# Optimization experiments

Measured on AMD Instinct MI355X. Metric: run time of the kernel, lower is better.

Reference implementation:

```python
import jax, jax.numpy as jnp
import numpy as np

HEADS = 8
DIM_HEAD = 64
SCALE = DIM_HEAD ** (-0.5)


def setup_inputs() -> dict:
    key = jax.random.key(0)
    k1, k2, k3, k4 = jax.random.split(key, 4)
    B, H, W, n, dim = 2, 64, 64, 8, 512
    inner = HEADS * DIM_HEAD  # 512
    x = jax.random.normal(k1, (B, H, W, n, dim), dtype=jnp.float32)
    mask = jax.random.uniform(k2, (B, H, W, 1, n, n), dtype=jnp.float32)
    w_qkv = jax.random.normal(k3, (dim, 3 * inner), dtype=jnp.float32) * 0.02
    w_out = jax.random.normal(k4, (inner, dim), dtype=jnp.float32) * 0.02
    b_out = jnp.zeros((dim,), dtype=jnp.float32)
    return {"x": x, "mask": mask, "w_qkv": w_qkv, "w_out": w_out, "b_out": b_out}


def reference(x, mask, w_qkv, w_out, b_out):
    B, H, W, n, dim = x.shape
    inner = HEADS * DIM_HEAD
    qkv = x @ w_qkv  # [B,H,W,n,3*inner]
    q, k, v = jnp.split(qkv, 3, axis=-1)

    def to_heads(t):
        # 'B H W n (h d) -> B H W h n d'
        t = t.reshape(B, H, W, n, HEADS, DIM_HEAD)
        return jnp.swapaxes(t, 3, 4)

    q, k, v = to_heads(q), to_heads(k), to_heads(v)
    dots = jnp.einsum('bxyhnd,bxyhmd->bxyhnm', q, k) * SCALE
    dots = dots * mask  # multiplicative mask pre-softmax
    attn = jax.nn.softmax(dots, axis=-1)
    out = jnp.einsum('bxyhnm,bxyhmd->bxyhnd', attn, v)
    # 'B H W h n d -> B H W n (h d)'
    out = jnp.swapaxes(out, 3, 4).reshape(B, H, W, n, inner)
    return out @ w_out + b_out
```

## Files before the change

### kernel.cpp

```cpp
#include <hip/hip_runtime.h>
#include <hip/hip_bf16.h>

#define NROWS 65536
#define DIM   512
#define SCALE_ 0.125f

typedef short bf16x8 __attribute__((ext_vector_type(8)));
typedef unsigned short u16x8 __attribute__((ext_vector_type(8)));
typedef float f32x4 __attribute__((ext_vector_type(4)));

__device__ __forceinline__ unsigned short f2bf(float f) {
  union { float f; unsigned u; } v; v.f = f;
  unsigned r = v.u + 0x7FFFu + ((v.u >> 16) & 1u);
  return (unsigned short)(r >> 16);
}

#define GLL16(gptr, lptr) \
  __builtin_amdgcn_global_load_lds((const __attribute__((address_space(1))) void*)(gptr), \
                                   (__attribute__((address_space(3))) void*)(lptr), 16, 0, 0)
#define VMCNT(n) asm volatile("s_waitcnt vmcnt(" #n ")" ::: "memory")
#define LGKM0    asm volatile("s_waitcnt lgkmcnt(0)" ::: "memory")

__global__ void prep_kernel(const float* __restrict__ x,
                            const float* __restrict__ wqkv,
                            const float* __restrict__ wout,
                            unsigned short* __restrict__ xb,
                            unsigned short* __restrict__ wqkvT,
                            unsigned short* __restrict__ woutT) {
  if (blockIdx.x < 16384) {
    size_t i = ((size_t)blockIdx.x * 256 + threadIdx.x) * 8;
    float4 a = *(const float4*)(x + i);
    float4 b = *(const float4*)(x + i + 4);
    u16x8 p;
    p[0] = f2bf(a.x); p[1] = f2bf(a.y); p[2] = f2bf(a.z); p[3] = f2bf(a.w);
    p[4] = f2bf(b.x); p[5] = f2bf(b.y); p[6] = f2bf(b.z); p[7] = f2bf(b.w);
    *(u16x8*)(xb + i) = p;
  } else {
    int idx = (blockIdx.x - 16384) * 256 + threadIdx.x;
    if (idx < 1536 * 512) {
      int j = idx >> 9, c = idx & 511;
      wqkvT[idx] = f2bf(wqkv[(size_t)c * 1536 + j]);
    } else {
      int k2 = idx - 1536 * 512;
      int n = k2 >> 9, c = k2 & 511;
      woutT[k2] = f2bf(wout[(size_t)c * 512 + n]);
    }
  }
}

__global__ __launch_bounds__(256, 2)
void qkv_attn_kernel(const unsigned short* __restrict__ xb,
                     const float* __restrict__ mask,
                     const unsigned short* __restrict__ wqkvT,
                     unsigned short* __restrict__ attn_out) {
  __shared__ __align__(16) unsigned char smem[62464];

  const int t = threadIdx.x;
  const int lane = t & 63, wave = t >> 6;
  const int wm = wave >> 1, wn = wave & 1;
  const int fr = lane & 15, fq = lane >> 4;
  const int l8 = lane >> 3;
  const int cswz = ((lane & 7) ^ l8) * 8;

  const int per = gridDim.x >> 3;
  const int lin = (blockIdx.x & 7) * per + (blockIdx.x >> 3);
  const int mtile = lin >> 3, head = lin & 7;
  const int r0 = mtile * 128;

  f32x4 acc[4][6];
  const f32x4 z4 = {0.f, 0.f, 0.f, 0.f};
  #pragma unroll
  for (int m = 0; m < 4; ++m)
    #pragma unroll
    for (int n = 0; n < 6; ++n) acc[m][n] = z4;

  auto LOAD_A = [&](bf16x8 (&a)[8], int kt2) {
    const unsigned short* g = xb + (size_t)(r0 + wm * 64 + fr) * 512 + kt2 * 64 + fq * 8;
    #pragma unroll
    for (int m = 0; m < 4; ++m)
      #pragma unroll
      for (int kk = 0; kk < 2; ++kk)
        a[m * 2 + kk] = *(const bf16x8*)(g + (size_t)m * 16 * 512 + kk * 32);
  };
  auto STAGE_B = [&](int buf, int kt2) {
    unsigned char* base = smem + buf * 24576;
    const unsigned short* gB = wqkvT + kt2 * 64 + cswz;
    #pragma unroll
    for (int i = 0; i < 6; ++i) {
      int c = wave * 6 + i;
      int n = c * 8 + l8;
      int jg = ((n >> 6) << 9) + head * 64 + (n & 63);
      GLL16(gB + (size_t)jg * 512, base + c * 1024);
    }
  };
  auto COMPUTE = [&](int buf, bf16x8 (&a)[8]) {
    unsigned char* Bb = smem + buf * 24576;
    #pragma unroll
    for (int kk = 0; kk < 2; ++kk) {
      const unsigned ko = ((unsigned)(kk * 64 + fq * 16)) ^ (((unsigned)(fr & 7)) << 4);
      bf16x8 b[6];
      #pragma unroll
      for (int n = 0; n < 6; ++n)
        b[n] = *(const bf16x8*)(Bb + (unsigned)(wn * 96 + n * 16 + fr) * 128 + ko);
      #pragma unroll
      for (int m = 0; m < 4; ++m)
        #pragma unroll
        for (int n = 0; n < 6; ++n)
          acc[m][n] = __builtin_amdgcn_mfma_f32_16x16x32_bf16(a[m * 2 + kk], b[n], acc[m][n], 0, 0, 0);
    }
  };

  bf16x8 aA[8], aB[8];
  LOAD_A(aA, 0);
  STAGE_B(0, 0);
  #pragma unroll
  for (int kt = 0; kt < 8; ++kt) {
    bf16x8 (&aCur)[8] = (kt & 1) ? aB : aA;
    bf16x8 (&aNxt)[8] = (kt & 1) ? aA : aB;
    if (kt < 7) {
      LOAD_A(aNxt, kt + 1);
      STAGE_B((kt + 1) & 1, kt + 1);
      VMCNT(11);
    } else {
      VMCNT(0);
    }
    __builtin_amdgcn_s_barrier();
    COMPUTE(kt & 1, aCur);
    __builtin_amdgcn_s_barrier();
  }

  unsigned short* Qs = (unsigned short*)smem;
  unsigned short* Ks = (unsigned short*)(smem + 16384);
  unsigned short* VT = (unsigned short*)(smem + 32768);
  unsigned short* Pl = (unsigned short*)(smem + 52224);

  float mreg[2][4];
  #pragma unroll
  for (int pp = 0; pp < 2; ++pp) {
    int pair = wave * 2 + pp;
    #pragma unroll
    for (int r = 0; r < 4; ++r) {
      int row = fq * 4 + r;
      int Pg = mtile * 16 + pair * 2 + (row >> 3);
      mreg[pp][r] = mask[(size_t)Pg * 64 + (row & 7) * 8 + (fr & 7)];
    }
  }

  {
    int d = t >> 2, q = t & 3;
    ushort4 z; z.x = 0; z.y = 0; z.z = 0; z.w = 0;
    *(ushort4*)(VT + d * 152 + 128 + q * 4) = z;
  }
  #pragma unroll
  for (int n = 0; n < 6; ++n) {
    int col = wn * 96 + n * 16 + fr;
    #pragma unroll
    for (int m = 0; m < 4; ++m) {
      if (col < 128) {
        unsigned short* T = (col < 64) ? Qs : Ks;
        unsigned cc = (unsigned)(col & 63);
        #pragma unroll
        for (int r = 0; r < 4; ++r) {
          int row = wm * 64 + m * 16 + fq * 4 + r;
          unsigned byte = (unsigned)row * 128 + ((cc * 2) ^ (((unsigned)(row & 7)) << 4));
          *(unsigned short*)((unsigned char*)T + byte) = f2bf(acc[m][n][r]);
        }
      } else {
        int d = col - 128;
        ushort4 p;
        p.x = f2bf(acc[m][n][0]); p.y = f2bf(acc[m][n][1]);
        p.z = f2bf(acc[m][n][2]); p.w = f2bf(acc[m][n][3]);
        *(ushort4*)(VT + d * 152 + (wm * 64 + m * 16 + fq * 4)) = p;
      }
    }
  }
  __syncthreads();

  #pragma unroll
  for (int pp = 0; pp < 2; ++pp) {
    const int pair = wave * 2 + pp;
    const unsigned rbyte = (unsigned)(pair * 16 + fr) * 128;
    const unsigned xrp = ((unsigned)(fr & 7)) << 4;
    f32x4 s = {0.f, 0.f, 0.f, 0.f};
    #pragma unroll
    for (int kk = 0; kk < 2; ++kk) {
      const unsigned ko = ((unsigned)(kk * 64 + fq * 16)) ^ xrp;
      bf16x8 qf = *(const bf16x8*)((unsigned char*)Qs + rbyte + ko);
      bf16x8 kf = *(const bf16x8*)((unsigned char*)Ks + rbyte + ko);
      s = __builtin_amdgcn_mfma_f32_16x16x32_bf16(qf, kf, s, 0, 0, 0);
    }
    float p4[4];
    #pragma unroll
    for (int r = 0; r < 4; ++r) {
      int row = fq * 4 + r;
      bool valid = (row >> 3) == (fr >> 3);
      p4[r] = valid ? s[r] * SCALE_ * mreg[pp][r] : -3.0e38f;
    }
    #pragma unroll
    for (int r = 0; r < 4; ++r) {
      float v = p4[r];
      float mx = v;
      mx = fmaxf(mx, __shfl_xor(mx, 1));
      mx = fmaxf(mx, __shfl_xor(mx, 2));
      mx = fmaxf(mx, __shfl_xor(mx, 4));
      float e = __expf(v - mx);
      float sm = e;
      sm += __shfl_xor(sm, 1);
      sm += __shfl_xor(sm, 2);
      sm += __shfl_xor(sm, 4);
      p4[r] = e / sm;
    }
    #pragma unroll
    for (int r = 0; r < 4; ++r) {
      int row = fq * 4 + r;
      bool valid = (row >> 3) == (fr >> 3);
      Pl[pair * 640 + row * 40 + fr] = valid ? f2bf(p4[r]) : (unsigned short)0;
      Pl[pair * 640 + row * 40 + 16 + fr] = 0;
    }
    #pragma unroll
    for (int dblk = 0; dblk < 4; ++dblk) {
      bf16x8 af = *(const bf16x8*)((unsigned char*)VT +
                    (unsigned)(dblk * 16 + fr) * 304 + (unsigned)(pair * 32 + fq * 16));
      bf16x8 bf = *(const bf16x8*)((unsigned char*)Pl +
                    (unsigned)pair * 1280 + (unsigned)fr * 80 + (unsigned)fq * 16);
      f32x4 o = {0.f, 0.f, 0.f, 0.f};
      o = __builtin_amdgcn_mfma_f32_16x16x32_bf16(af, bf, o, 0, 0, 0);
      ushort4 pk;
      pk.x = f2bf(o[0]); pk.y = f2bf(o[1]); pk.z = f2bf(o[2]); pk.w = f2bf(o[3]);
      *(ushort4*)(attn_out + (size_t)(r0 + pair * 16 + fr) * 512 +
                  head * 64 + dblk * 16 + fq * 4) = pk;
    }
  }
}

__global__ __launch_bounds__(256, 2)
void outproj_kernel(const unsigned short* __restrict__ attn,
                    const unsigned short* __restrict__ woutT,
                    const float* __restrict__ bias,
                    float* __restrict__ out) {
  __shared__ __align__(16) unsigned char smem[65536];
  const int t = threadIdx.x;
  const int lane = t & 63, wave = t >> 6;
  const int wm = wave >> 1, wn = wave & 1;
  const int fr = lane & 15, fq = lane >> 4;
  const int l8 = lane >> 3;
  const int cswz = ((lane & 7) ^ l8) * 8;

  const int per = gridDim.x >> 3;
  const int lin = (blockIdx.x & 7) * per + (blockIdx.x >> 3);
  const int mtile = lin >> 2, nt = lin & 3;
  const int r0 = mtile * 128, n0 = nt * 128;

  f32x4 acc[4][4];
  const f32x4 z4 = {0.f, 0.f, 0.f, 0.f};
  #pragma unroll
  for (int m = 0; m < 4; ++m)
    #pragma unroll
    for (int n = 0; n < 4; ++n) acc[m][n] = z4;

  auto STAGE = [&](int buf, int kt2) {
    unsigned char* base = smem + buf * 32768;
    const int k0 = kt2 * 64;
    const unsigned short* gA = attn  + (size_t)(r0 + l8) * 512 + k0 + cswz;
    const unsigned short* gB = woutT + (size_t)(n0 + l8) * 512 + k0 + cswz;
    #pragma unroll
    for (int i = 0; i < 4; ++i) {
      int c = wave * 4 + i;
      GLL16(gA + (size_t)c * 8 * 512, base + c * 1024);
      GLL16(gB + (size_t)c * 8 * 512, base + 16384 + c * 1024);
    }
  };

  STAGE(0, 0);
  VMCNT(0);
  __syncthreads();
  int cur = 0;

  for (int kt = 0; kt < 8; ++kt) {
    if (kt < 7) STAGE(cur ^ 1, kt + 1);
    unsigned char* Ab = smem + cur * 32768;
    unsigned char* Bb = Ab + 16384;
    const unsigned xr = ((unsigned)(fr & 7)) << 4;
    #pragma unroll
    for (int kk = 0; kk < 2; ++kk) {
      const unsigned ko = ((unsigned)(kk * 64 + fq * 16)) ^ xr;
      bf16x8 a[4], b[4];
      #pragma unroll
      for (int m = 0; m < 4; ++m)
        a[m] = *(const bf16x8*)(Ab + (unsigned)(wm * 64 + m * 16 + fr) * 128 + ko);
      #pragma unroll
      for (int n = 0; n < 4; ++n)
        b[n] = *(const bf16x8*)(Bb + (unsigned)(wn * 64 + n * 16 + fr) * 128 + ko);
      #pragma unroll
      for (int m = 0; m < 4; ++m)
        #pragma unroll
        for (int n = 0; n < 4; ++n)
          acc[m][n] = __builtin_amdgcn_mfma_f32_16x16x32_bf16(a[m], b[n], acc[m][n], 0, 0, 0);
    }
    VMCNT(0);
    __syncthreads();
    cur ^= 1;
  }
  #pragma unroll
  for (int n = 0; n < 4; ++n) {
    int col = n0 + wn * 64 + n * 16 + fr;
    float bv = bias[col];
    #pragma unroll
    for (int m = 0; m < 4; ++m) {
      #pragma unroll
      for (int j = 0; j < 4; ++j) {
        int row = r0 + wm * 64 + m * 16 + fq * 4 + j;
        out[(size_t)row * 512 + col] = acc[m][n][j] + bv;
      }
    }
  }
}

extern "C" void kernel_launch(void* const* d_in, const int* in_sizes, int n_in,
                              void* d_out, int out_size, void* d_ws, size_t ws_size,
                              hipStream_t stream) {
  const float* x    = (const float*)d_in[0];
  const float* mask = (const float*)d_in[1];
  const float* wqkv = (const float*)d_in[2];
  const float* wout = (const float*)d_in[3];
  const float* bias = (const float*)d_in[4];
  float* out = (float*)d_out;

  unsigned char* ws = (unsigned char*)d_ws;
  unsigned short* attn  = (unsigned short*)ws;
  unsigned short* wqkvT = (unsigned short*)(ws + 67108864);
  unsigned short* woutT = (unsigned short*)(ws + 67108864 + 1572864);
  unsigned short* xb    = (unsigned short*)(ws + 67108864 + 1572864 + 524288);

  prep_kernel<<<20480, 256, 0, stream>>>(x, wqkv, wout, xb, wqkvT, woutT);
  qkv_attn_kernel<<<4096, 256, 0, stream>>>(xb, mask, wqkvT, attn);
  outproj_kernel<<<2048, 256, 0, stream>>>(attn, woutT, bias, out);
}
```

Measured before the change: 279.8 us.

## Stage QKV A tiles through LDS and coalesce output GEMM epilogue via shared memory

In the fused QKV+attention kernel, the A operand (x in bf16) now goes to LDS through global_load_lds alongside B, replacing direct per-lane register loads with register double-buffering. Shared memory grows to 80 KB, which may limit occupancy to one or two blocks per CU. The mask loads move earlier so their latency overlaps the GEMM. The output-projection epilogue now goes through a swizzled LDS tile, so each row is written with coalesced float4 stores plus vectorized bias, in place of scattered scalar stores.

```diff
diff --git a/kernel.cpp b/kernel.cpp
--- a/kernel.cpp
+++ b/kernel.cpp
@@ -18,8 +18,7 @@
 #define GLL16(gptr, lptr) \
   __builtin_amdgcn_global_load_lds((const __attribute__((address_space(1))) void*)(gptr), \
                                    (__attribute__((address_space(3))) void*)(lptr), 16, 0, 0)
-#define VMCNT(n) asm volatile("s_waitcnt vmcnt(" #n ")" ::: "memory")
-#define LGKM0    asm volatile("s_waitcnt lgkmcnt(0)" ::: "memory")
+#define VMCNT0 asm volatile("s_waitcnt vmcnt(0)" ::: "memory")
 
 __global__ void prep_kernel(const float* __restrict__ x,
                             const float* __restrict__ wqkv,
@@ -53,7 +52,7 @@
                      const float* __restrict__ mask,
                      const unsigned short* __restrict__ wqkvT,
                      unsigned short* __restrict__ attn_out) {
-  __shared__ __align__(16) unsigned char smem[62464];
+  __shared__ __align__(16) unsigned char smem[81920];
 
   const int t = threadIdx.x;
   const int lane = t & 63, wave = t >> 6;
@@ -67,6 +66,18 @@
   const int mtile = lin >> 3, head = lin & 7;
   const int r0 = mtile * 128;
 
+  float mreg[2][4];
+  #pragma unroll
+  for (int pp = 0; pp < 2; ++pp) {
+    int pair = wave * 2 + pp;
+    #pragma unroll
+    for (int r = 0; r < 4; ++r) {
+      int row = fq * 4 + r;
+      int Pg = mtile * 16 + pair * 2 + (row >> 3);
+      mreg[pp][r] = mask[(size_t)Pg * 64 + (row & 7) * 8 + (fr & 7)];
+    }
+  }
+
   f32x4 acc[4][6];
   const f32x4 z4 = {0.f, 0.f, 0.f, 0.f};
   #pragma unroll
@@ -74,31 +85,42 @@
     #pragma unroll
     for (int n = 0; n < 6; ++n) acc[m][n] = z4;
 
-  auto LOAD_A = [&](bf16x8 (&a)[8], int kt2) {
-    const unsigned short* g = xb + (size_t)(r0 + wm * 64 + fr) * 512 + kt2 * 64 + fq * 8;
-    #pragma unroll
-    for (int m = 0; m < 4; ++m)
-      #pragma unroll
-      for (int kk = 0; kk < 2; ++kk)
-        a[m * 2 + kk] = *(const bf16x8*)(g + (size_t)m * 16 * 512 + kk * 32);
-  };
-  auto STAGE_B = [&](int buf, int kt2) {
-    unsigned char* base = smem + buf * 24576;
-    const unsigned short* gB = wqkvT + kt2 * 64 + cswz;
+  auto STAGE = [&](int buf, int kt2) {
+    unsigned char* base = smem + buf * 40960;
+    const int k0 = kt2 * 64;
+    const unsigned short* gA = xb + (size_t)(r0 + l8) * 512 + k0 + cswz;
+    #pragma unroll
+    for (int i = 0; i < 4; ++i) {
+      int c = wave * 4 + i;
+      GLL16(gA + (size_t)c * 8 * 512, base + c * 1024);
+    }
+    const unsigned short* gB = wqkvT + k0 + cswz;
     #pragma unroll
     for (int i = 0; i < 6; ++i) {
       int c = wave * 6 + i;
       int n = c * 8 + l8;
       int jg = ((n >> 6) << 9) + head * 64 + (n & 63);
-      GLL16(gB + (size_t)jg * 512, base + c * 1024);
+      GLL16(gB + (size_t)jg * 512, base + 16384 + c * 1024);
     }
   };
-  auto COMPUTE = [&](int buf, bf16x8 (&a)[8]) {
-    unsigned char* Bb = smem + buf * 24576;
+
+  STAGE(0, 0);
+  VMCNT0;
+  __syncthreads();
+  int cur = 0;
+
+  for (int kt = 0; kt < 8; ++kt) {
+    if (kt < 7) STAGE(cur ^ 1, kt + 1);
+    unsigned char* Ab = smem + cur * 40960;
+    unsigned char* Bb = Ab + 16384;
+    const unsigned xr = ((unsigned)(fr & 7)) << 4;
     #pragma unroll
     for (int kk = 0; kk < 2; ++kk) {
-      const unsigned ko = ((unsigned)(kk * 64 + fq * 16)) ^ (((unsigned)(fr & 7)) << 4);
-      bf16x8 b[6];
+      const unsigned ko = ((unsigned)(kk * 64 + fq * 16)) ^ xr;
+      bf16x8 a[4], b[6];
+      #pragma unroll
+      for (int m = 0; m < 4; ++m)
+        a[m] = *(const bf16x8*)(Ab + (unsigned)(wm * 64 + m * 16 + fr) * 128 + ko);
       #pragma unroll
       for (int n = 0; n < 6; ++n)
         b[n] = *(const bf16x8*)(Bb + (unsigned)(wn * 96 + n * 16 + fr) * 128 + ko);
@@ -106,45 +128,17 @@
       for (int m = 0; m < 4; ++m)
         #pragma unroll
         for (int n = 0; n < 6; ++n)
-          acc[m][n] = __builtin_amdgcn_mfma_f32_16x16x32_bf16(a[m * 2 + kk], b[n], acc[m][n], 0, 0, 0);
-    }
-  };
-
-  bf16x8 aA[8], aB[8];
-  LOAD_A(aA, 0);
-  STAGE_B(0, 0);
-  #pragma unroll
-  for (int kt = 0; kt < 8; ++kt) {
-    bf16x8 (&aCur)[8] = (kt & 1) ? aB : aA;
-    bf16x8 (&aNxt)[8] = (kt & 1) ? aA : aB;
-    if (kt < 7) {
-      LOAD_A(aNxt, kt + 1);
-      STAGE_B((kt + 1) & 1, kt + 1);
-      VMCNT(11);
-    } else {
-      VMCNT(0);
-    }
-    __builtin_amdgcn_s_barrier();
-    COMPUTE(kt & 1, aCur);
-    __builtin_amdgcn_s_barrier();
+          acc[m][n] = __builtin_amdgcn_mfma_f32_16x16x32_bf16(a[m], b[n], acc[m][n], 0, 0, 0);
+    }
+    VMCNT0;
+    __syncthreads();
+    cur ^= 1;
   }
 
   unsigned short* Qs = (unsigned short*)smem;
   unsigned short* Ks = (unsigned short*)(smem + 16384);
   unsigned short* VT = (unsigned short*)(smem + 32768);
   unsigned short* Pl = (unsigned short*)(smem + 52224);
-
-  float mreg[2][4];
-  #pragma unroll
-  for (int pp = 0; pp < 2; ++pp) {
-    int pair = wave * 2 + pp;
-    #pragma unroll
-    for (int r = 0; r < 4; ++r) {
-      int row = fq * 4 + r;
-      int Pg = mtile * 16 + pair * 2 + (row >> 3);
-      mreg[pp][r] = mask[(size_t)Pg * 64 + (row & 7) * 8 + (fr & 7)];
-    }
-  }
 
   {
     int d = t >> 2, q = t & 3;
@@ -272,7 +266,7 @@
   };
 
   STAGE(0, 0);
-  VMCNT(0);
+  VMCNT0;
   __syncthreads();
   int cur = 0;
 
@@ -297,22 +291,37 @@
         for (int n = 0; n < 4; ++n)
           acc[m][n] = __builtin_amdgcn_mfma_f32_16x16x32_bf16(a[m], b[n], acc[m][n], 0, 0, 0);
     }
-    VMCNT(0);
+    VMCNT0;
     __syncthreads();
     cur ^= 1;
   }
+
+  float* Cl = (float*)smem;
   #pragma unroll
   for (int n = 0; n < 4; ++n) {
-    int col = n0 + wn * 64 + n * 16 + fr;
-    float bv = bias[col];
+    int colh = wn * 16 + n * 4 + (fr >> 2);
+    int cb = fr & 3;
     #pragma unroll
     for (int m = 0; m < 4; ++m) {
       #pragma unroll
       for (int j = 0; j < 4; ++j) {
-        int row = r0 + wm * 64 + m * 16 + fq * 4 + j;
-        out[(size_t)row * 512 + col] = acc[m][n][j] + bv;
+        int row = wm * 64 + m * 16 + fq * 4 + j;
+        unsigned ps = (unsigned)(colh ^ (row & 31));
+        Cl[(unsigned)row * 128 + ps * 4 + cb] = acc[m][n][j];
       }
     }
+  }
+  __syncthreads();
+  const int slot = t & 31;
+  const float4 bv = *(const float4*)(bias + n0 + slot * 4);
+  #pragma unroll
+  for (int it = 0; it < 16; ++it) {
+    int row = it * 8 + (t >> 5);
+    unsigned ps = (unsigned)(slot ^ (row & 31));
+    float4 v = *(const float4*)(Cl + (unsigned)row * 128 + ps * 4);
+    float4 o;
+    o.x = v.x + bv.x; o.y = v.y + bv.y; o.z = v.z + bv.z; o.w = v.w + bv.w;
+    *(float4*)(out + (size_t)(r0 + row) * 512 + n0 + slot * 4) = o;
   }
 }
 
```

Result: faster. 254.9 us (-8.9%).
